# Performance work log

Measured on AMD Instinct MI355X. Metric: run time of the kernel, lower is better.

The kernel has to match this reference:

```python
import jax, jax.numpy as jnp
import numpy as np

NUM_PIDS = 5532
NUM_CQ = 5000
D = 256
N = 8192
OIM_SCALAR = 30.0
IGNORE = 5554  # hardcoded ignore_index in the original F.cross_entropy call


def _l2norm(x):
    return x / jnp.linalg.norm(x, axis=-1, keepdims=True)


def setup_inputs() -> dict:
    key = jax.random.key(0)
    k0, k1, k2, k3, k4, k5 = jax.random.split(key, 6)
    inputs = _l2norm(jax.random.normal(k0, (N, D), dtype=jnp.float32))
    label = jax.random.randint(k1, (N,), 0, NUM_PIDS)
    label = jnp.where(jax.random.uniform(k2, (N,)) < 0.1, IGNORE, label).astype(jnp.int64)
    ious = jax.random.uniform(k3, (N,), minval=0.5, maxval=1.0, dtype=jnp.float32)
    lut = _l2norm(jax.random.normal(k4, (NUM_PIDS, D), dtype=jnp.float32))
    cq = _l2norm(jax.random.normal(k5, (NUM_CQ, D), dtype=jnp.float32))
    reliability = 0.5 * jnp.ones((NUM_PIDS + NUM_CQ,), dtype=jnp.float32)
    return {"inputs": inputs, "label": label, "ious": ious,
            "lut": lut, "cq": cq, "reliability": reliability}


def reference(inputs, label, ious, lut, cq, reliability):
    # OIM.forward: logits = [inputs @ lut.T | inputs @ cq.T] * reliability, then * oim_scalar
    bank = jnp.concatenate([lut, cq], axis=0)              # [num_pids+num_cq, D]
    logits = (inputs @ bank.T) * reliability[None, :] * OIM_SCALAR  # [N, L]
    # F.cross_entropy(projected, label, ignore_index=5554): mean over non-ignored rows
    logp = jax.nn.log_softmax(logits, axis=-1)
    valid = label != IGNORE
    safe = jnp.where(valid, label, 0)
    nll = -jnp.take_along_axis(logp, safe[:, None], axis=1)[:, 0]
    n_valid = jnp.maximum(jnp.sum(valid.astype(jnp.float32)), 1.0)
    loss = jnp.sum(jnp.where(valid, nll, 0.0)) / n_valid
    return loss
```

## Files before the change

### kernel.cpp

```cpp
#include <hip/hip_runtime.h>
#include <stdint.h>

#define NROWS 8192
#define DDIM 256
#define NPIDS 5532
#define NCQ 5000
#define LCOLS 10532
#define IGNORE_IDX 5554
#define NT 83
#define LPAD (NT * 128)
#define NSPLIT 8
#define NPARTS (NSPLIT * 2)
#define PADCOLS (LPAD - LCOLS)
#define TSTEP (NSPLIT * 65536)
#define OIM_SCALE 30.0f
#define LOG2E 1.4426950408889634f
#define LN2f 0.6931471805599453f

using f32x4 = __attribute__((ext_vector_type(4))) float;
using bf16x8 = __attribute__((ext_vector_type(8))) __bf16;
using ushort8 = __attribute__((ext_vector_type(8))) unsigned short;

#define WS_INBF 0u
#define WS_BANK 4194304u
#define WS_PARTS 9633792u
#define WS_RLOGIT 10158080u
#define WS_BLK 10190848u
#define WS_NEED 10191104u

__device__ __forceinline__ unsigned short f2bf(float f) {
  union { float f; uint32_t u; } v; v.f = f;
  uint32_t u = v.u;
  uint32_t r = (u + 0x7FFFu + ((u >> 16) & 1u)) >> 16;
  return (unsigned short)r;
}

__device__ __forceinline__ void async16(const void* g, void* l) {
  __builtin_amdgcn_global_load_lds(
      (const __attribute__((address_space(1))) uint32_t*)g,
      (__attribute__((address_space(3))) uint32_t*)l, 16, 0, 0);
}

__global__ void prep_label_kernel(const float* __restrict__ inputs,
                                  const int* __restrict__ label,
                                  const float* __restrict__ lut,
                                  const float* __restrict__ cq,
                                  const float* __restrict__ rel,
                                  unsigned short* __restrict__ in2,
                                  unsigned short* __restrict__ bank3,
                                  float* __restrict__ rowlogit) {
  {
    const int lane = threadIdx.x & 63;
    const int wvl = threadIdx.x >> 6;
    const int row = blockIdx.x * 4 + wvl;
    const int l = label[row];
    float out = 0.0f;
    if (l != IGNORE_IDX && l >= 0 && l < LCOLS) {
      const float* bk = (l < NPIDS) ? (lut + (size_t)l * DDIM)
                                    : (cq + (size_t)(l - NPIDS) * DDIM);
      f32x4 a = *(const f32x4*)(inputs + (size_t)row * DDIM + lane * 4);
      f32x4 b = *(const f32x4*)(bk + lane * 4);
      float d = a[0] * b[0] + a[1] * b[1] + a[2] * b[2] + a[3] * b[3];
#pragma unroll
      for (int m = 1; m < 64; m <<= 1) d += __shfl_xor(d, m);
      out = OIM_SCALE * rel[l] * d;
    }
    if (lane == 0) rowlogit[row] = out;
  }
  const int GIN = NROWS * (DDIM / 8);
  const int GBK = LPAD * (DDIM / 8);
  const int total = GIN + GBK;
  for (int d = blockIdx.x * blockDim.x + threadIdx.x; d < total;
       d += gridDim.x * blockDim.x) {
    const float* src = nullptr;
    unsigned short* dst;
    float scale = 1.0f;
    bool zero = false;
    if (d < GIN) {
      const int R = ((d >> 9) << 4) | (d & 15);
      const int c8 = (((d >> 6) & 7) << 2) | ((d >> 4) & 3);
      src = inputs + R * DDIM + c8 * 8;
      dst = in2 + (size_t)d * 8;
    } else {
      const int b = d - GIN;
      const int R = ((b >> 12) << 7) | (((b >> 9) & 7) << 4) | (b & 15);
      const int c8 = (((b >> 6) & 7) << 2) | ((b >> 4) & 3);
      dst = bank3 + (size_t)b * 8;
      if (R < NPIDS) src = lut + (size_t)R * DDIM + c8 * 8;
      else if (R < LCOLS) src = cq + (size_t)(R - NPIDS) * DDIM + c8 * 8;
      else zero = true;
      if (!zero) scale = OIM_SCALE * LOG2E * rel[R];
    }
    ushort8 o = {0, 0, 0, 0, 0, 0, 0, 0};
    if (!zero) {
      const f32x4* s4 = (const f32x4*)src;
      f32x4 v0 = s4[0], v1 = s4[1];
      o[0] = f2bf(v0[0] * scale); o[1] = f2bf(v0[1] * scale);
      o[2] = f2bf(v0[2] * scale); o[3] = f2bf(v0[3] * scale);
      o[4] = f2bf(v1[0] * scale); o[5] = f2bf(v1[1] * scale);
      o[6] = f2bf(v1[2] * scale); o[7] = f2bf(v1[3] * scale);
    }
    *(ushort8*)dst = o;
  }
}

#define STG(PP)                                                           \
  do {                                                                    \
    char* _d = dT + (((PP) + 2) & 3) * 16384;                             \
    async16(sgP, _d);                                                     \
    async16(sgP + 32768, _d + 8192);                                      \
    sgP += ((PP) == 1) ? (TSTEP - 6144) : 2048;                           \
  } while (0)

#define PHASE(PP, VMN)                                                    \
  do {                                                                    \
    asm volatile("s_waitcnt vmcnt(" #VMN ")" ::: "memory");               \
    asm volatile("s_barrier" ::: "memory");                               \
    const char* _c = rB + (PP) * 16384;                                   \
    bf16x8 bF[4][2];                                                      \
    _Pragma("unroll") for (int _ni = 0; _ni < 4; ++_ni)                   \
      _Pragma("unroll") for (int _kl = 0; _kl < 2; ++_kl)                 \
        bF[_ni][_kl] = *(const bf16x8*)(_c + _ni * 2048 + _kl * 1024);    \
    asm volatile("s_waitcnt lgkmcnt(0)" ::: "memory");                    \
    __builtin_amdgcn_sched_barrier(0);                                    \
    __builtin_amdgcn_s_setprio(1);                                        \
    _Pragma("unroll") for (int _kl = 0; _kl < 2; ++_kl)                   \
      _Pragma("unroll") for (int _mi = 0; _mi < 4; ++_mi)                 \
        _Pragma("unroll") for (int _ni = 0; _ni < 4; ++_ni)               \
          acc[_mi][_ni] = __builtin_amdgcn_mfma_f32_16x16x32_bf16(        \
              aR[_mi][(PP) * 2 + _kl], bF[_ni][_kl],                      \
              ((PP) == 0 && _kl == 0) ? vzero : acc[_mi][_ni], 0, 0, 0);  \
    __builtin_amdgcn_s_setprio(0);                                        \
  } while (0)

__global__ __launch_bounds__(512, 2) void oim_main_kernel(
    const unsigned short* __restrict__ in2,
    const unsigned short* __restrict__ bank3,
    float* __restrict__ parts) {
  extern __shared__ char ring[];
  const int tid = threadIdx.x;
  const int lane = tid & 63;
  const int wv = tid >> 6;
  const int wrow = wv >> 1;
  const int wcol = wv & 1;
  const int ql = lane & 15;
  const int h = lane >> 4;

  const int bid = blockIdx.x;
  const int sp = bid & 7;
  const int bm = bid >> 3;
  const int ntiles = (sp < 3) ? 11 : 10;

  bf16x8 aR[4][8];
  {
    const char* ab =
        (const char*)in2 + (size_t)(bm * 16 + wrow * 4) * 8192 + lane * 16;
#pragma unroll
    for (int mi = 0; mi < 4; ++mi)
#pragma unroll
      for (int kk = 0; kk < 8; ++kk)
        aR[mi][kk] = *(const bf16x8*)(ab + mi * 8192 + kk * 1024);
  }
  const int rowb = bm * 256 + wrow * 64 + h * 4;

  asm volatile("" ::: "memory");

  const char* sgT = (const char*)bank3 + (size_t)sp * 65536 +
                    (tid >> 7) * 8192 + (tid & 127) * 16;
  char* dT = ring + tid * 16;

  async16(sgT, dT);
  async16(sgT + 32768, dT + 8192);
  asm volatile("" ::: "memory");
  async16(sgT + 2048, dT + 16384);
  async16(sgT + 2048 + 32768, dT + 16384 + 8192);
  asm volatile("" ::: "memory");
  const char* sgP = sgT + 4096;

  const char* rB = ring + (wcol * 4) * 2048 + lane * 16;

  const f32x4 vzero = {0.f, 0.f, 0.f, 0.f};
  f32x4 acc[4][4];
  float se[4][4];
#pragma unroll
  for (int a = 0; a < 4; ++a)
#pragma unroll
    for (int b = 0; b < 4; ++b) se[a][b] = 0.f;

  for (int t = 0; t < ntiles - 1; ++t) {
    STG(0); PHASE(0, 4);
    STG(1); PHASE(1, 4);
    STG(2); PHASE(2, 4);
    STG(3); PHASE(3, 4);
#pragma unroll
    for (int mi = 0; mi < 4; ++mi)
#pragma unroll
      for (int ni = 0; ni < 4; ++ni)
#pragma unroll
        for (int r = 0; r < 4; ++r)
          se[mi][r] += __builtin_amdgcn_exp2f(acc[mi][ni][r]);
  }
  STG(0); PHASE(0, 4);
  STG(1); PHASE(1, 4);
  PHASE(2, 2);
  PHASE(3, 0);
#pragma unroll
  for (int mi = 0; mi < 4; ++mi)
#pragma unroll
    for (int ni = 0; ni < 4; ++ni)
#pragma unroll
      for (int r = 0; r < 4; ++r)
        se[mi][r] += __builtin_amdgcn_exp2f(acc[mi][ni][r]);

#pragma unroll
  for (int mi = 0; mi < 4; ++mi)
#pragma unroll
    for (int r = 0; r < 4; ++r) {
      float v = se[mi][r];
      v += __shfl_xor(v, 1);
      v += __shfl_xor(v, 2);
      v += __shfl_xor(v, 4);
      v += __shfl_xor(v, 8);
      se[mi][r] = v;
    }
  if (ql == 0) {
    const int part = sp * 2 + wcol;
#pragma unroll
    for (int mi = 0; mi < 4; ++mi) {
      f32x4 o = {se[mi][0], se[mi][1], se[mi][2], se[mi][3]};
      *(f32x4*)(parts + (size_t)part * NROWS + rowb + mi * 16) = o;
    }
  }
}

__global__ void reduce1_kernel(const float* __restrict__ parts,
                               const float* __restrict__ rowlogit,
                               const int* __restrict__ label,
                               float* __restrict__ blk) {
  const int r = blockIdx.x * 256 + threadIdx.x;
  float s = 0.0f, c = 0.0f;
  if (label[r] != IGNORE_IDX) {
    float tot = 0.0f;
#pragma unroll
    for (int p = 0; p < NPARTS; ++p) tot += parts[p * NROWS + r];
    tot -= (float)PADCOLS;
    s = LN2f * __builtin_log2f(tot) - rowlogit[r];
    c = 1.0f;
  }
#pragma unroll
  for (int m = 1; m < 64; m <<= 1) {
    s += __shfl_xor(s, m);
    c += __shfl_xor(c, m);
  }
  __shared__ float ss[4], sc[4];
  const int wv = threadIdx.x >> 6, lane = threadIdx.x & 63;
  if (lane == 0) { ss[wv] = s; sc[wv] = c; }
  __syncthreads();
  if (threadIdx.x == 0) {
    blk[blockIdx.x * 2 + 0] = ss[0] + ss[1] + ss[2] + ss[3];
    blk[blockIdx.x * 2 + 1] = sc[0] + sc[1] + sc[2] + sc[3];
  }
}

__global__ void reduce2_kernel(const float* __restrict__ blk,
                               float* __restrict__ out) {
  const int lane = threadIdx.x;
  float s = (lane < 32) ? blk[lane * 2 + 0] : 0.0f;
  float c = (lane < 32) ? blk[lane * 2 + 1] : 0.0f;
#pragma unroll
  for (int m = 1; m < 32; m <<= 1) {
    s += __shfl_xor(s, m);
    c += __shfl_xor(c, m);
  }
  if (lane == 0) out[0] = s / fmaxf(c, 1.0f);
}

extern "C" void kernel_launch(void* const* d_in, const int* in_sizes, int n_in,
                              void* d_out, int out_size, void* d_ws,
                              size_t ws_size, hipStream_t stream) {
  const float* inputs = (const float*)d_in[0];
  const int* label = (const int*)d_in[1];
  const float* lut = (const float*)d_in[3];
  const float* cq = (const float*)d_in[4];
  const float* rel = (const float*)d_in[5];
  float* out = (float*)d_out;
  char* ws = (char*)d_ws;
  if (ws_size < WS_NEED) return;

  unsigned short* in2 = (unsigned short*)(ws + WS_INBF);
  unsigned short* bank3 = (unsigned short*)(ws + WS_BANK);
  float* parts = (float*)(ws + WS_PARTS);
  float* rowlogit = (float*)(ws + WS_RLOGIT);
  float* blk = (float*)(ws + WS_BLK);

  hipFuncSetAttribute((const void*)oim_main_kernel,
                      hipFuncAttributeMaxDynamicSharedMemorySize, 65536);

  prep_label_kernel<<<dim3(2048), dim3(256), 0, stream>>>(
      inputs, label, lut, cq, rel, in2, bank3, rowlogit);
  oim_main_kernel<<<dim3(256), dim3(512), 65536, stream>>>(in2, bank3, parts);
  reduce1_kernel<<<dim3(32), dim3(256), 0, stream>>>(parts, rowlogit, label,
                                                     blk);
  reduce2_kernel<<<dim3(1), dim3(64), 0, stream>>>(blk, out);
}
```

Baseline: 57.25 us.

## Switch main GEMM from bf16 to fp8 e4m3 MFMA with rescaled operands

Quantizes the inputs (scaled by 4) and the reliability-scaled bank to fp8 e4m3 in the prep kernel, and runs the logits GEMM with fp8 MFMA instructions. Packed layouts, LDS ring size, staging offsets and wait counts are rewritten to match the halved byte width. The aim is to halve memory traffic and LDS use and to raise MFMA throughput. The cost is much lower logit precision: with a scale near 43 the exponentiated sums may drift from the reference, and the e4m3 conversion is done in software. Launch bounds also drop the min-blocks hint from 2 to 1.

```diff
diff --git a/kernel.cpp b/kernel.cpp
--- a/kernel.cpp
+++ b/kernel.cpp
@@ -12,27 +12,50 @@
 #define NSPLIT 8
 #define NPARTS (NSPLIT * 2)
 #define PADCOLS (LPAD - LCOLS)
-#define TSTEP (NSPLIT * 65536)
+#define BTILE 32768
+#define TSTEP (NSPLIT * BTILE)
 #define OIM_SCALE 30.0f
 #define LOG2E 1.4426950408889634f
 #define LN2f 0.6931471805599453f
+#define SA 4.0f
 
 using f32x4 = __attribute__((ext_vector_type(4))) float;
-using bf16x8 = __attribute__((ext_vector_type(8))) __bf16;
-using ushort8 = __attribute__((ext_vector_type(8))) unsigned short;
-
-#define WS_INBF 0u
-#define WS_BANK 4194304u
-#define WS_PARTS 9633792u
-#define WS_RLOGIT 10158080u
-#define WS_BLK 10190848u
-#define WS_NEED 10191104u
-
-__device__ __forceinline__ unsigned short f2bf(float f) {
-  union { float f; uint32_t u; } v; v.f = f;
-  uint32_t u = v.u;
-  uint32_t r = (u + 0x7FFFu + ((u >> 16) & 1u)) >> 16;
-  return (unsigned short)r;
+using i64x2 = __attribute__((ext_vector_type(2))) long;
+using uchar16 = __attribute__((ext_vector_type(16))) unsigned char;
+
+#define WS_INF8 0u
+#define WS_BANK 2097152u
+#define WS_PARTS 4816896u
+#define WS_RLOGIT 5341184u
+#define WS_BLK 5373952u
+#define WS_NEED 5374208u
+
+__device__ __forceinline__ unsigned char f2e4m3(float x) {
+  union { float f; uint32_t u; } v; v.f = x;
+  const uint32_t s = (v.u >> 24) & 0x80u;
+  const int eb = (int)((v.u >> 23) & 0xFFu);
+  const uint32_t m = v.u & 0x7FFFFFu;
+  const int e = eb - 127;
+  if (eb == 255 || e >= 9) return (unsigned char)(s | 0x7Eu);
+  if (e >= -6) {
+    uint32_t keep = m >> 20;
+    const uint32_t rest = m & 0xFFFFFu;
+    keep += (rest > 0x80000u) || (rest == 0x80000u && (keep & 1u));
+    uint32_t ee = (uint32_t)(e + 7);
+    if (keep == 8u) { keep = 0u; ee += 1u; }
+    if (ee > 15u || (ee == 15u && keep == 7u))
+      return (unsigned char)(s | 0x7Eu);
+    return (unsigned char)(s | (ee << 3) | keep);
+  }
+  if (e < -10) return (unsigned char)s;
+  const int sh = 14 - e;
+  const uint32_t full = 0x800000u | m;
+  uint32_t q = full >> sh;
+  const uint32_t rem = full & ((1u << sh) - 1u);
+  const uint32_t half = 1u << (sh - 1);
+  q += (rem > half) || (rem == half && (q & 1u));
+  if (q >= 8u) return (unsigned char)(s | 8u);
+  return (unsigned char)(s | q);
 }
 
 __device__ __forceinline__ void async16(const void* g, void* l) {
@@ -46,8 +69,8 @@
                                   const float* __restrict__ lut,
                                   const float* __restrict__ cq,
                                   const float* __restrict__ rel,
-                                  unsigned short* __restrict__ in2,
-                                  unsigned short* __restrict__ bank3,
+                                  unsigned char* __restrict__ inf8,
+                                  unsigned char* __restrict__ bank8,
                                   float* __restrict__ rowlogit) {
   {
     const int lane = threadIdx.x & 63;
@@ -67,75 +90,85 @@
     }
     if (lane == 0) rowlogit[row] = out;
   }
-  const int GIN = NROWS * (DDIM / 8);
-  const int GBK = LPAD * (DDIM / 8);
+  const int GIN = NROWS * (DDIM / 16);
+  const int GBK = LPAD * (DDIM / 16);
   const int total = GIN + GBK;
   for (int d = blockIdx.x * blockDim.x + threadIdx.x; d < total;
        d += gridDim.x * blockDim.x) {
     const float* src = nullptr;
-    unsigned short* dst;
+    unsigned char* dst;
     float scale = 1.0f;
     bool zero = false;
     if (d < GIN) {
-      const int R = ((d >> 9) << 4) | (d & 15);
-      const int c8 = (((d >> 6) & 7) << 2) | ((d >> 4) & 3);
-      src = inputs + R * DDIM + c8 * 8;
-      dst = in2 + (size_t)d * 8;
+      const int rest = d & 255;
+      const int L = rest & 63;
+      const int R = ((d >> 8) << 4) | (L & 15);
+      const int k0 = ((rest >> 6) << 6) | ((L >> 4) << 3);
+      src = inputs + (size_t)R * DDIM + k0;
+      dst = inf8 + (size_t)d * 16;
+      scale = SA;
     } else {
       const int b = d - GIN;
-      const int R = ((b >> 12) << 7) | (((b >> 9) & 7) << 4) | (b & 15);
-      const int c8 = (((b >> 6) & 7) << 2) | ((b >> 4) & 3);
-      dst = bank3 + (size_t)b * 8;
-      if (R < NPIDS) src = lut + (size_t)R * DDIM + c8 * 8;
-      else if (R < LCOLS) src = cq + (size_t)(R - NPIDS) * DDIM + c8 * 8;
+      const int rest = b & 2047;
+      const int rest2 = rest & 255;
+      const int L = rest2 & 63;
+      const int C = ((b >> 11) << 7) | (((rest >> 8) & 7) << 4) | (L & 15);
+      const int k0 = ((rest2 >> 6) << 6) | ((L >> 4) << 3);
+      dst = bank8 + (size_t)b * 16;
+      if (C < NPIDS) src = lut + (size_t)C * DDIM + k0;
+      else if (C < LCOLS) src = cq + (size_t)(C - NPIDS) * DDIM + k0;
       else zero = true;
-      if (!zero) scale = OIM_SCALE * LOG2E * rel[R];
-    }
-    ushort8 o = {0, 0, 0, 0, 0, 0, 0, 0};
+      if (!zero) scale = OIM_SCALE * LOG2E * rel[C] * (1.0f / SA);
+    }
+    uchar16 o = {0};
     if (!zero) {
       const f32x4* s4 = (const f32x4*)src;
-      f32x4 v0 = s4[0], v1 = s4[1];
-      o[0] = f2bf(v0[0] * scale); o[1] = f2bf(v0[1] * scale);
-      o[2] = f2bf(v0[2] * scale); o[3] = f2bf(v0[3] * scale);
-      o[4] = f2bf(v1[0] * scale); o[5] = f2bf(v1[1] * scale);
-      o[6] = f2bf(v1[2] * scale); o[7] = f2bf(v1[3] * scale);
-    }
-    *(ushort8*)dst = o;
-  }
-}
-
-#define STG(PP)                                                           \
+      f32x4 u0 = s4[0], u1 = s4[1];
+      f32x4 w0 = s4[8], w1 = s4[9];
+#pragma unroll
+      for (int j = 0; j < 4; ++j) {
+        o[j] = f2e4m3(u0[j] * scale);
+        o[j + 4] = f2e4m3(u1[j] * scale);
+        o[j + 8] = f2e4m3(w0[j] * scale);
+        o[j + 12] = f2e4m3(w1[j] * scale);
+      }
+    }
+    *(uchar16*)dst = o;
+  }
+}
+
+#define STG(ADV)                                                          \
   do {                                                                    \
-    char* _d = dT + (((PP) + 2) & 3) * 16384;                             \
-    async16(sgP, _d);                                                     \
-    async16(sgP + 32768, _d + 8192);                                      \
-    sgP += ((PP) == 1) ? (TSTEP - 6144) : 2048;                           \
+    async16(sgP + (tid >> 6) * 4096 + (tid & 63) * 16,                    \
+            ring + roS + tid * 16);                                       \
+    sgP += (ADV);                                                         \
+    roS += 8192; if (roS == 32768) roS = 0;                               \
   } while (0)
 
 #define PHASE(PP, VMN)                                                    \
   do {                                                                    \
     asm volatile("s_waitcnt vmcnt(" #VMN ")" ::: "memory");               \
     asm volatile("s_barrier" ::: "memory");                               \
-    const char* _c = rB + (PP) * 16384;                                   \
-    bf16x8 bF[4][2];                                                      \
+    const char* _c = rB + roN;                                            \
+    i64x2 bF[4];                                                          \
     _Pragma("unroll") for (int _ni = 0; _ni < 4; ++_ni)                   \
-      _Pragma("unroll") for (int _kl = 0; _kl < 2; ++_kl)                 \
-        bF[_ni][_kl] = *(const bf16x8*)(_c + _ni * 2048 + _kl * 1024);    \
+      bF[_ni] = *(const i64x2*)(_c + _ni * 1024);                         \
     asm volatile("s_waitcnt lgkmcnt(0)" ::: "memory");                    \
     __builtin_amdgcn_sched_barrier(0);                                    \
     __builtin_amdgcn_s_setprio(1);                                        \
     _Pragma("unroll") for (int _kl = 0; _kl < 2; ++_kl)                   \
       _Pragma("unroll") for (int _mi = 0; _mi < 4; ++_mi)                 \
         _Pragma("unroll") for (int _ni = 0; _ni < 4; ++_ni)               \
-          acc[_mi][_ni] = __builtin_amdgcn_mfma_f32_16x16x32_bf16(        \
-              aR[_mi][(PP) * 2 + _kl], bF[_ni][_kl],                      \
+          acc[_mi][_ni] = __builtin_amdgcn_mfma_f32_16x16x32_fp8_fp8(     \
+              aR[_mi][(PP)][_kl], bF[_ni][_kl],                           \
               ((PP) == 0 && _kl == 0) ? vzero : acc[_mi][_ni], 0, 0, 0);  \
     __builtin_amdgcn_s_setprio(0);                                        \
+    roN += 8192; if (roN == 32768) roN = 0;                               \
   } while (0)
 
-__global__ __launch_bounds__(512, 2) void oim_main_kernel(
-    const unsigned short* __restrict__ in2,
-    const unsigned short* __restrict__ bank3,
+__global__ __launch_bounds__(512, 1) void oim_main_kernel(
+    const unsigned char* __restrict__ inf8,
+    const unsigned char* __restrict__ bank8,
     float* __restrict__ parts) {
   extern __shared__ char ring[];
   const int tid = threadIdx.x;
@@ -151,33 +184,30 @@
   const int bm = bid >> 3;
   const int ntiles = (sp < 3) ? 11 : 10;
 
-  bf16x8 aR[4][8];
+  i64x2 aR[4][4];
   {
     const char* ab =
-        (const char*)in2 + (size_t)(bm * 16 + wrow * 4) * 8192 + lane * 16;
+        (const char*)inf8 + (size_t)(bm * 16 + wrow * 4) * 4096 + lane * 16;
 #pragma unroll
     for (int mi = 0; mi < 4; ++mi)
 #pragma unroll
-      for (int kk = 0; kk < 8; ++kk)
-        aR[mi][kk] = *(const bf16x8*)(ab + mi * 8192 + kk * 1024);
+      for (int kp = 0; kp < 4; ++kp)
+        aR[mi][kp] = *(const i64x2*)(ab + mi * 4096 + kp * 1024);
   }
   const int rowb = bm * 256 + wrow * 64 + h * 4;
 
   asm volatile("" ::: "memory");
 
-  const char* sgT = (const char*)bank3 + (size_t)sp * 65536 +
-                    (tid >> 7) * 8192 + (tid & 127) * 16;
-  char* dT = ring + tid * 16;
-
-  async16(sgT, dT);
-  async16(sgT + 32768, dT + 8192);
-  asm volatile("" ::: "memory");
-  async16(sgT + 2048, dT + 16384);
-  async16(sgT + 2048 + 32768, dT + 16384 + 8192);
-  asm volatile("" ::: "memory");
-  const char* sgP = sgT + 4096;
-
-  const char* rB = ring + (wcol * 4) * 2048 + lane * 16;
+  const char* sgT = (const char*)bank8 + (size_t)sp * BTILE;
+#pragma unroll
+  for (int p = 0; p < 2; ++p)
+    async16(sgT + (tid >> 6) * 4096 + p * 1024 + (tid & 63) * 16,
+            ring + p * 8192 + tid * 16);
+  const char* sgP = sgT + 2048;
+  int roS = 16384;
+  int roN = 0;
+
+  const char* rB = ring + wcol * 4096 + lane * 16;
 
   const f32x4 vzero = {0.f, 0.f, 0.f, 0.f};
   f32x4 acc[4][4];
@@ -188,10 +218,10 @@
     for (int b = 0; b < 4; ++b) se[a][b] = 0.f;
 
   for (int t = 0; t < ntiles - 1; ++t) {
-    STG(0); PHASE(0, 4);
-    STG(1); PHASE(1, 4);
-    STG(2); PHASE(2, 4);
-    STG(3); PHASE(3, 4);
+    STG(1024);          PHASE(0, 2);
+    STG(TSTEP - 3072);  PHASE(1, 2);
+    STG(1024);          PHASE(2, 2);
+    STG(1024);          PHASE(3, 2);
 #pragma unroll
     for (int mi = 0; mi < 4; ++mi)
 #pragma unroll
@@ -200,9 +230,9 @@
         for (int r = 0; r < 4; ++r)
           se[mi][r] += __builtin_amdgcn_exp2f(acc[mi][ni][r]);
   }
-  STG(0); PHASE(0, 4);
-  STG(1); PHASE(1, 4);
-  PHASE(2, 2);
+  STG(1024); PHASE(0, 2);
+  STG(1024); PHASE(1, 2);
+  PHASE(2, 1);
   PHASE(3, 0);
 #pragma unroll
   for (int mi = 0; mi < 4; ++mi)
@@ -287,18 +317,18 @@
   char* ws = (char*)d_ws;
   if (ws_size < WS_NEED) return;
 
-  unsigned short* in2 = (unsigned short*)(ws + WS_INBF);
-  unsigned short* bank3 = (unsigned short*)(ws + WS_BANK);
+  unsigned char* inf8 = (unsigned char*)(ws + WS_INF8);
+  unsigned char* bank8 = (unsigned char*)(ws + WS_BANK);
   float* parts = (float*)(ws + WS_PARTS);
   float* rowlogit = (float*)(ws + WS_RLOGIT);
   float* blk = (float*)(ws + WS_BLK);
 
   hipFuncSetAttribute((const void*)oim_main_kernel,
-                      hipFuncAttributeMaxDynamicSharedMemorySize, 65536);
+                      hipFuncAttributeMaxDynamicSharedMemorySize, 32768);
 
   prep_label_kernel<<<dim3(2048), dim3(256), 0, stream>>>(
-      inputs, label, lut, cq, rel, in2, bank3, rowlogit);
-  oim_main_kernel<<<dim3(256), dim3(512), 65536, stream>>>(in2, bank3, parts);
+      inputs, label, lut, cq, rel, inf8, bank8, rowlogit);
+  oim_main_kernel<<<dim3(256), dim3(512), 32768, stream>>>(inf8, bank8, parts);
   reduce1_kernel<<<dim3(32), dim3(256), 0, stream>>>(parts, rowlogit, label,
                                                      blk);
   reduce2_kernel<<<dim3(1), dim3(64), 0, stream>>>(blk, out);
```

Result: faster. 54.49 us (-4.8%).
